# Kernel optimization log

Hardware: AMD Instinct MI355X
Metric: run time of the kernel (lower is better)

The kernel has to match this reference:

```python
import jax, jax.numpy as jnp
import numpy as np

N_CELLS, N_CLASSES, N_GENES, N_EDGES, HID = 100000, 50, 500, 600000, 8
NEG_SLOPE = 0.2  # GATv2Conv default negative_slope


def setup_inputs() -> dict:
    key = jax.random.key(0)
    ks = jax.random.split(key, 10)
    X = jax.random.normal(ks[0], (N_CELLS, N_GENES), jnp.float32)
    Mu = jax.random.normal(ks[1], (N_CLASSES, N_GENES), jnp.float32)
    # variances must be strictly positive
    Var = jax.random.uniform(ks[2], (N_CLASSES, N_GENES), jnp.float32) + 0.5
    W = 0.1 * jax.random.normal(ks[3], (N_CELLS, N_CLASSES), jnp.float32)
    S = 1.0 + 0.05 * jax.random.normal(ks[4], (N_CELLS, 1), jnp.float32)
    edge_index = jax.random.randint(ks[5], (2, N_EDGES), 0, N_CELLS, jnp.int32)
    sc = 1.0 / np.sqrt(N_GENES)
    lin_l_w = sc * jax.random.normal(ks[6], (HID, N_GENES), jnp.float32)
    lin_l_b = jnp.zeros((HID,), jnp.float32)
    lin_r_w = sc * jax.random.normal(ks[7], (HID, N_GENES), jnp.float32)
    lin_r_b = jnp.zeros((HID,), jnp.float32)
    att = jax.random.normal(ks[8], (HID,), jnp.float32) / np.sqrt(HID)
    return dict(X=X, Mu=Mu, Var=Var, W=W, S=S, edge_index=edge_index,
                lin_l_w=lin_l_w, lin_l_b=lin_l_b,
                lin_r_w=lin_r_w, lin_r_b=lin_r_b, att=att)


def _forward(X, Mu, Var, W, S, lin_l_w, lin_l_b, lin_r_w, lin_r_b, att, edge_index):
    N = X.shape[0]
    P = jax.nn.softmax(W, axis=1)  # [N, C]

    # Gaussian log-likelihood term.
    # F[n,c] = -0.5 * sum_g (X[n,g] - Mu[c,g]*S[n])^2 / Var[c,g]
    # Expanded into GEMMs (algebraically identical, avoids the [N,C,G] intermediate):
    invV = 1.0 / Var                          # [C, G]
    t1 = (X * X) @ invV.T                     # [N, C]  sum_g X^2/Var
    t2 = X @ (Mu * invV).T                    # [N, C]  sum_g X*Mu/Var
    t3 = jnp.sum(Mu * Mu * invV, axis=1)      # [C]     sum_g Mu^2/Var
    Fmat = -0.5 * (t1 - 2.0 * S * t2 + (S * S) * t3[None, :])  # [N, C]
    ll_prot = jnp.sum(P * Fmat) / N

    # GATv2 attention coefficients (heads=1, add_self_loops=False).
    gl = X @ lin_l_w.T + lin_l_b              # [N, HID]  lin_l (source side)
    gr = X @ lin_r_w.T + lin_r_b              # [N, HID]  lin_r (target side)
    src, dst = edge_index[0], edge_index[1]
    e = jax.nn.leaky_relu(gl[src] + gr[dst], NEG_SLOPE)  # [E, HID]
    score = e @ att                                       # [E]
    # segment softmax over destination nodes
    m = jax.ops.segment_max(score, dst, num_segments=N)
    ex = jnp.exp(score - m[dst])
    denom = jax.ops.segment_sum(ex, dst, num_segments=N)
    alpha = ex / denom[dst]                               # [E]

    ce_space = -jnp.sum(P[src] * alpha[:, None] * jnp.log(P[dst] + 1e-8)) / N
    return ll_prot, ce_space, P


def reference(X, Mu, Var, W, S, edge_index, lin_l_w, lin_l_b, lin_r_w, lin_r_b, att):
    return _forward(X, Mu, Var, W, S, lin_l_w, lin_l_b, lin_r_w, lin_r_b, att, edge_index)
```

## Files before the change

kernel.cpp:

```cpp
#include <hip/hip_runtime.h>
#include <math.h>

#define N_CELLS   100000
#define N_CLASSES 50
#define N_GENES   500
#define N_EDGES   600000
#define HID       8
#define NKT       8
#define NB_FUSED  1563
#define NB_CE     391

typedef __attribute__((ext_vector_type(4))) float f32x4;
typedef __attribute__((ext_vector_type(8))) short bf16x8;

static const size_t OFF_BF    = 0;
static const size_t OFF_T3    = 147456;
static const size_t OFF_GLR   = 147712;
static const size_t OFF_SCORE = 6547712;
static const size_t OFF_MSEG  = 8947712;
static const size_t OFF_DENOM = 9347712;
static const size_t OFF_NUMER = 9747712;
static const size_t OFF_LLP   = 10147712;
static const size_t OFF_CEP   = 10153968;
static const size_t ZERO_BEG  = OFF_MSEG;
static const size_t ZERO_BYTES= 10147712 - 8947712;

__device__ __forceinline__ ushort f2bf(float f) {
    union { float f; unsigned u; } v; v.f = f;
    unsigned r = v.u + 0x7fffu + ((v.u >> 16) & 1u);
    return (ushort)(r >> 16);
}

__device__ __forceinline__ unsigned cvt_pk_bf16(float lo, float hi) {
    unsigned r;
    asm("v_cvt_pk_bf16_f32 %0, %1, %2" : "=v"(r) : "v"(lo), "v"(hi));
    return r;
}

__device__ __forceinline__ void gload16(const void* g, void* l) {
    __builtin_amdgcn_global_load_lds(
        (const __attribute__((address_space(1))) unsigned int*)g,
        (__attribute__((address_space(3))) unsigned int*)l,
        16, 0, 0);
}

__global__ __launch_bounds__(256) void k_prepB(const float* __restrict__ Var,
                                               const float* __restrict__ Mu,
                                               const float* __restrict__ wl,
                                               const float* __restrict__ wr,
                                               ushort* __restrict__ Bf) {
    int id = blockIdx.x * 256 + threadIdx.x;
    float v = 0.f;
    if (id < 65536) {
        int e    = id & 7;
        int lane = (id >> 3) & 63;
        int j    = (id >> 9) & 15;
        int kt   = id >> 13;
        int t    = j >> 1, ss = j & 1;
        int s    = kt * 2 + ss;
        int k    = s * 32 + ((lane >> 4) << 3) + e;
        int c    = (t & 3) * 16 + (lane & 15);
        if (k < N_GENES && c < N_CLASSES)
            v = (t < 4) ? 1.0f / Var[c * N_GENES + k]
                        : Mu[c * N_GENES + k] / Var[c * N_GENES + k];
    } else {
        int rem  = id - 65536;
        int e    = rem & 7;
        int lane = (rem >> 3) & 63;
        int s    = rem >> 9;
        int k    = s * 32 + ((lane >> 4) << 3) + e;
        int h    = lane & 15;
        if (k < N_GENES)
            v = (h < HID) ? wl[h * N_GENES + k] : wr[(h - HID) * N_GENES + k];
    }
    Bf[id] = f2bf(v);
}

__global__ void k_t3(const float* __restrict__ Var, const float* __restrict__ Mu,
                     float* __restrict__ t3) {
    int c = blockIdx.x;
    int lane = threadIdx.x;
    float s = 0.f;
    for (int g = lane; g < N_GENES; g += 64) {
        float m = Mu[c * N_GENES + g];
        s += m * m / Var[c * N_GENES + g];
    }
    #pragma unroll
    for (int off = 32; off; off >>= 1) s += __shfl_xor(s, off);
    if (lane == 0) t3[c] = s;
}

__global__ __launch_bounds__(256) void k_softmax(const float* __restrict__ W,
                                                 float* __restrict__ P) {
    int wid  = (blockIdx.x * 256 + threadIdx.x) >> 6;
    int lane = threadIdx.x & 63;
    if (wid >= N_CELLS) return;
    float w = (lane < N_CLASSES) ? W[(size_t)wid * N_CLASSES + lane] : -__builtin_inff();
    float m = w;
    #pragma unroll
    for (int off = 32; off; off >>= 1) m = fmaxf(m, __shfl_xor(m, off));
    float e = (lane < N_CLASSES) ? expf(w - m) : 0.f;
    float s = e;
    #pragma unroll
    for (int off = 32; off; off >>= 1) s += __shfl_xor(s, off);
    if (lane < N_CLASSES) P[(size_t)wid * N_CLASSES + lane] = e / s;
}

__global__ __launch_bounds__(256, 1) void k_fused(const float* __restrict__ X,
                                                  const float* __restrict__ S,
                                                  const float* __restrict__ P,
                                                  const ushort* __restrict__ Bf,
                                                  const float* __restrict__ t3,
                                                  const float* __restrict__ bl,
                                                  const float* __restrict__ br,
                                                  float* __restrict__ glr,
                                                  float* __restrict__ llp) {
    __shared__ float  ldsA[2][4][16][16][4];
    __shared__ ushort ldsB[2][16][64][8];
    int tid  = threadIdx.x;
    int lane = tid & 63;
    int wv   = tid >> 6;
    int lhi  = lane >> 4;
    int slot = lane & 15;
    int rbase = blockIdx.x * 64;
    const char* Xc  = (const char*)X;
    const char* Bfc = (const char*)Bf;
    const bf16x8* Bg8 = (const bf16x8*)(Bf + 65536);

    int arow = rbase + wv * 16 + (lane & 15);
    if (arow > N_CELLS - 1) arow = N_CELLS - 1;
    float sv  = S[arow];
    float m2s = -2.0f * sv;

    const f32x4 zz = {0.f, 0.f, 0.f, 0.f};
    f32x4 acc1[4], acc2[4], acc3;
    #pragma unroll
    for (int ct = 0; ct < 4; ++ct) { acc1[ct] = zz; acc2[ct] = zz; }
    acc3 = zz;

    #pragma unroll
    for (int i = 0; i < 4; ++i) {
        int rloc = i * 4 + lhi;
        int row  = rbase + wv * 16 + rloc; if (row > N_CELLS - 1) row = N_CELLS - 1;
        int gi   = slot ^ (rloc & 7); if (gi > 124) gi = 124;
        gload16(Xc + (size_t)row * 2000 + (size_t)gi * 16, &ldsA[0][wv][i * 4][0][0]);
    }
    #pragma unroll
    for (int i = 0; i < 4; ++i) {
        int j = wv * 4 + i;
        gload16(Bfc + (size_t)j * 1024 + (size_t)lane * 16, &ldsB[0][j][0][0]);
    }

    int cur = 0;
    for (int kt = 0; kt < NKT; ++kt) {
        __syncthreads();
        if (kt < NKT - 1) {
            int nxt = cur ^ 1;
            #pragma unroll
            for (int i = 0; i < 4; ++i) {
                int rloc = i * 4 + lhi;
                int row  = rbase + wv * 16 + rloc; if (row > N_CELLS - 1) row = N_CELLS - 1;
                int gi   = (kt + 1) * 16 + (slot ^ (rloc & 7)); if (gi > 124) gi = 124;
                gload16(Xc + (size_t)row * 2000 + (size_t)gi * 16, &ldsA[nxt][wv][i * 4][0][0]);
            }
            #pragma unroll
            for (int i = 0; i < 4; ++i) {
                int j = wv * 4 + i;
                gload16(Bfc + (size_t)(kt + 1) * 16384 + (size_t)j * 1024 + (size_t)lane * 16,
                        &ldsB[nxt][j][0][0]);
            }
        }
        const bf16x8* BL = (const bf16x8*)&ldsB[cur][0][0][0];
        #pragma unroll
        for (int ks = 0; ks < 2; ++ks) {
            int rloc = lane & 15, key = rloc & 7;
            int g8   = ks * 8 + lhi * 2;
            f32x4 xa = *(const f32x4*)&ldsA[cur][wv][rloc][g8 ^ key][0];
            f32x4 xb = *(const f32x4*)&ldsA[cur][wv][rloc][(g8 + 1) ^ key][0];
            union { bf16x8 v; unsigned u[4]; } a1, a2;
            a1.u[0] = cvt_pk_bf16(xa[0] * xa[0], xa[1] * xa[1]);
            a1.u[1] = cvt_pk_bf16(xa[2] * xa[2], xa[3] * xa[3]);
            a1.u[2] = cvt_pk_bf16(xb[0] * xb[0], xb[1] * xb[1]);
            a1.u[3] = cvt_pk_bf16(xb[2] * xb[2], xb[3] * xb[3]);
            a2.u[0] = cvt_pk_bf16(m2s * xa[0], m2s * xa[1]);
            a2.u[1] = cvt_pk_bf16(m2s * xa[2], m2s * xa[3]);
            a2.u[2] = cvt_pk_bf16(m2s * xb[0], m2s * xb[1]);
            a2.u[3] = cvt_pk_bf16(m2s * xb[2], m2s * xb[3]);
            bf16x8 bg = Bg8[(size_t)(kt * 2 + ks) * 64 + lane];
            #pragma unroll
            for (int ct = 0; ct < 4; ++ct)
                acc1[ct] = __builtin_amdgcn_mfma_f32_16x16x32_bf16(a1.v, BL[(ct * 2 + ks) * 64 + lane], acc1[ct], 0, 0, 0);
            #pragma unroll
            for (int ct = 0; ct < 4; ++ct)
                acc2[ct] = __builtin_amdgcn_mfma_f32_16x16x32_bf16(a2.v, BL[((4 + ct) * 2 + ks) * 64 + lane], acc2[ct], 0, 0, 0);
            acc3 = __builtin_amdgcn_mfma_f32_16x16x32_bf16(a2.v, bg, acc3, 0, 0, 0);
        }
        cur ^= 1;
    }

    int col = lane & 15;
    int rg  = lane >> 4;
    float bias = (col < HID) ? bl[col] : br[col - HID];
    float part = 0.f;
    #pragma unroll
    for (int r = 0; r < 4; ++r) {
        int row = rbase + wv * 16 + rg * 4 + r;
        if (row < N_CELLS) {
            float s2 = S[row];
            glr[(size_t)row * 16 + col] = acc3[r] / (-2.0f * s2) + bias;
            float ss = s2 * s2;
            #pragma unroll
            for (int ct = 0; ct < 4; ++ct) {
                int c = ct * 16 + col;
                if (c < N_CLASSES) {
                    float F = -0.5f * (acc1[ct][r] + acc2[ct][r] + ss * t3[c]);
                    part = fmaf(P[(size_t)row * N_CLASSES + c], F, part);
                }
            }
        }
    }
    #pragma unroll
    for (int off = 32; off; off >>= 1) part += __shfl_xor(part, off);
    float* wsum = (float*)&ldsA[0][0][0][0][0];
    __syncthreads();
    if (lane == 0) wsum[wv] = part;
    __syncthreads();
    if (tid == 0) llp[blockIdx.x] = wsum[0] + wsum[1] + wsum[2] + wsum[3];
}

__device__ __forceinline__ unsigned map_f32(float f) {
    int s = __float_as_int(f);
    return (s < 0) ? ~(unsigned)s : ((unsigned)s | 0x80000000u);
}
__device__ __forceinline__ float unmap_f32(unsigned u) {
    return (u & 0x80000000u) ? __int_as_float((int)(u & 0x7fffffffu))
                             : __int_as_float((int)~u);
}

__global__ __launch_bounds__(256) void k_score(const int* __restrict__ ei,
                                               const float* __restrict__ glr,
                                               const float* __restrict__ att,
                                               float* __restrict__ score,
                                               unsigned* __restrict__ mseg) {
    int e = blockIdx.x * 256 + threadIdx.x;
    if (e >= N_EDGES) return;
    int src = ei[e], dst = ei[N_EDGES + e];
    const float4* a = (const float4*)(glr + (size_t)src * 16);
    const float4* b = (const float4*)(glr + (size_t)dst * 16 + 8);
    float4 g0 = a[0], g1 = a[1], h0 = b[0], h1 = b[1];
    const float4* at = (const float4*)att;
    float4 a0 = at[0], a1 = at[1];
    float v, s = 0.f;
    v = g0.x + h0.x; v = v > 0.f ? v : 0.2f * v; s = fmaf(a0.x, v, s);
    v = g0.y + h0.y; v = v > 0.f ? v : 0.2f * v; s = fmaf(a0.y, v, s);
    v = g0.z + h0.z; v = v > 0.f ? v : 0.2f * v; s = fmaf(a0.z, v, s);
    v = g0.w + h0.w; v = v > 0.f ? v : 0.2f * v; s = fmaf(a0.w, v, s);
    v = g1.x + h1.x; v = v > 0.f ? v : 0.2f * v; s = fmaf(a1.x, v, s);
    v = g1.y + h1.y; v = v > 0.f ? v : 0.2f * v; s = fmaf(a1.y, v, s);
    v = g1.z + h1.z; v = v > 0.f ? v : 0.2f * v; s = fmaf(a1.z, v, s);
    v = g1.w + h1.w; v = v > 0.f ? v : 0.2f * v; s = fmaf(a1.w, v, s);
    score[e] = s;
    atomicMax(mseg + dst, map_f32(s));
}

__global__ __launch_bounds__(256) void k_edge2(const int* __restrict__ ei,
                                               const float* __restrict__ score,
                                               const unsigned* __restrict__ mseg,
                                               const float* __restrict__ P,
                                               float* __restrict__ denom,
                                               float* __restrict__ numer) {
    int t = blockIdx.x * 256 + threadIdx.x;
    int e = t >> 4;
    int q = t & 15;
    if (e >= N_EDGES) return;
    int src = ei[e], dst = ei[N_EDGES + e];
    float ex = expf(score[e] - unmap_f32(mseg[dst]));
    const float* Ps = P + (size_t)src * N_CLASSES;
    const float* Pd = P + (size_t)dst * N_CLASSES;
    float v = Ps[q]      * logf(Pd[q]      + 1e-8f)
            + Ps[q + 16] * logf(Pd[q + 16] + 1e-8f)
            + Ps[q + 32] * logf(Pd[q + 32] + 1e-8f);
    if (q < 2) v += Ps[q + 48] * logf(Pd[q + 48] + 1e-8f);
    v += __shfl_xor(v, 8); v += __shfl_xor(v, 4);
    v += __shfl_xor(v, 2); v += __shfl_xor(v, 1);
    if (q == 0) {
        atomicAdd(denom + dst, ex);
        atomicAdd(numer + dst, ex * v);
    }
}

__global__ __launch_bounds__(256) void k_ce(const float* __restrict__ denom,
                                            const float* __restrict__ numer,
                                            float* __restrict__ cep) {
    __shared__ float wsum[4];
    int n = blockIdx.x * 256 + threadIdx.x;
    float v = 0.f;
    if (n < N_CELLS) {
        float d = denom[n];
        v = (d > 0.f) ? numer[n] / d : 0.f;
    }
    #pragma unroll
    for (int off = 32; off; off >>= 1) v += __shfl_xor(v, off);
    if ((threadIdx.x & 63) == 0) wsum[threadIdx.x >> 6] = v;
    __syncthreads();
    if (threadIdx.x == 0) cep[blockIdx.x] = wsum[0] + wsum[1] + wsum[2] + wsum[3];
}

__global__ __launch_bounds__(256) void k_reduce(const float* __restrict__ llp,
                                                const float* __restrict__ cep,
                                                float* __restrict__ out) {
    __shared__ double l1[256], l2[256];
    int t = threadIdx.x;
    double s1 = 0.0, s2 = 0.0;
    for (int i = t; i < NB_FUSED; i += 256) s1 += (double)llp[i];
    for (int i = t; i < NB_CE; i += 256) s2 += (double)cep[i];
    l1[t] = s1; l2[t] = s2;
    __syncthreads();
    for (int off = 128; off; off >>= 1) {
        if (t < off) { l1[t] += l1[t + off]; l2[t] += l2[t + off]; }
        __syncthreads();
    }
    if (t == 0) {
        out[0] = (float)(l1[0] / (double)N_CELLS);
        out[1] = (float)(-l2[0] / (double)N_CELLS);
    }
}

extern "C" void kernel_launch(void* const* d_in, const int* in_sizes, int n_in,
                              void* d_out, int out_size, void* d_ws, size_t ws_size,
                              hipStream_t stream) {
    const float* X   = (const float*)d_in[0];
    const float* Mu  = (const float*)d_in[1];
    const float* Var = (const float*)d_in[2];
    const float* W   = (const float*)d_in[3];
    const float* S   = (const float*)d_in[4];
    const int*   ei  = (const int*)d_in[5];
    const float* wl  = (const float*)d_in[6];
    const float* bl  = (const float*)d_in[7];
    const float* wr  = (const float*)d_in[8];
    const float* br  = (const float*)d_in[9];
    const float* att = (const float*)d_in[10];
    float* out = (float*)d_out;
    char*  ws  = (char*)d_ws;

    ushort*   Bf    = (ushort*)(ws + OFF_BF);
    float*    t3    = (float*)(ws + OFF_T3);
    float*    glr   = (float*)(ws + OFF_GLR);
    float*    score = (float*)(ws + OFF_SCORE);
    unsigned* mseg  = (unsigned*)(ws + OFF_MSEG);
    float*    denom = (float*)(ws + OFF_DENOM);
    float*    numer = (float*)(ws + OFF_NUMER);
    float*    llp   = (float*)(ws + OFF_LLP);
    float*    cep   = (float*)(ws + OFF_CEP);
    float*    P     = out + 2;

    hipMemsetAsync(ws + ZERO_BEG, 0, ZERO_BYTES, stream);

    k_prepB  <<<288, 256, 0, stream>>>(Var, Mu, wl, wr, Bf);
    k_t3     <<<N_CLASSES, 64, 0, stream>>>(Var, Mu, t3);
    k_softmax<<<(N_CELLS * 64 + 255) / 256, 256, 0, stream>>>(W, P);
    k_fused  <<<NB_FUSED, 256, 0, stream>>>(X, S, P, Bf, t3, bl, br, glr, llp);
    k_score  <<<(N_EDGES + 255) / 256, 256, 0, stream>>>(ei, glr, att, score, mseg);
    k_edge2  <<<(N_EDGES * 16 + 255) / 256, 256, 0, stream>>>(ei, score, mseg, P, denom, numer);
    k_ce     <<<NB_CE, 256, 0, stream>>>(denom, numer, cep);
    k_reduce <<<1, 256, 0, stream>>>(llp, cep, out);
}
```

Baseline: 206.1 us.

## Process 32 rows per wave with single-buffered LDS and higher occupancy

Each wave now computes two 16-row tiles (128 rows per block, half as many blocks), so every B fragment read from LDS feeds two MFMAs. The double-buffered LDS prefetch is replaced by a single buffer with load-then-sync each k-step, and launch bounds now ask for 3 blocks per CU so concurrent blocks hide the load latency. The cost is no intra-block overlap of loads and compute, more accumulator registers per thread, and an extra barrier per iteration.

```diff
diff --git a/kernel.cpp b/kernel.cpp
--- a/kernel.cpp
+++ b/kernel.cpp
@@ -7,7 +7,7 @@
 #define N_EDGES   600000
 #define HID       8
 #define NKT       8
-#define NB_FUSED  1563
+#define NB_FUSED  782
 #define NB_CE     391
 
 typedef __attribute__((ext_vector_type(4))) float f32x4;
@@ -106,7 +106,7 @@
     if (lane < N_CLASSES) P[(size_t)wid * N_CLASSES + lane] = e / s;
 }
 
-__global__ __launch_bounds__(256, 1) void k_fused(const float* __restrict__ X,
+__global__ __launch_bounds__(256, 3) void k_fused(const float* __restrict__ X,
                                                   const float* __restrict__ S,
                                                   const float* __restrict__ P,
                                                   const ushort* __restrict__ Bf,
@@ -115,87 +115,91 @@
                                                   const float* __restrict__ br,
                                                   float* __restrict__ glr,
                                                   float* __restrict__ llp) {
-    __shared__ float  ldsA[2][4][16][16][4];
-    __shared__ ushort ldsB[2][16][64][8];
+    __shared__ float  ldsA[4][32][16][4];
+    __shared__ ushort ldsB[16][64][8];
+    __shared__ float  wsum[4];
     int tid  = threadIdx.x;
     int lane = tid & 63;
     int wv   = tid >> 6;
     int lhi  = lane >> 4;
     int slot = lane & 15;
-    int rbase = blockIdx.x * 64;
+    int rbase = blockIdx.x * 128 + wv * 32;
     const char* Xc  = (const char*)X;
     const char* Bfc = (const char*)Bf;
     const bf16x8* Bg8 = (const bf16x8*)(Bf + 65536);
 
-    int arow = rbase + wv * 16 + (lane & 15);
-    if (arow > N_CELLS - 1) arow = N_CELLS - 1;
-    float sv  = S[arow];
-    float m2s = -2.0f * sv;
+    int ar0 = rbase + slot;      if (ar0 > N_CELLS - 1) ar0 = N_CELLS - 1;
+    int ar1 = rbase + 16 + slot; if (ar1 > N_CELLS - 1) ar1 = N_CELLS - 1;
+    float m2s0 = -2.0f * S[ar0];
+    float m2s1 = -2.0f * S[ar1];
 
     const f32x4 zz = {0.f, 0.f, 0.f, 0.f};
-    f32x4 acc1[4], acc2[4], acc3;
-    #pragma unroll
-    for (int ct = 0; ct < 4; ++ct) { acc1[ct] = zz; acc2[ct] = zz; }
-    acc3 = zz;
-
-    #pragma unroll
-    for (int i = 0; i < 4; ++i) {
-        int rloc = i * 4 + lhi;
-        int row  = rbase + wv * 16 + rloc; if (row > N_CELLS - 1) row = N_CELLS - 1;
-        int gi   = slot ^ (rloc & 7); if (gi > 124) gi = 124;
-        gload16(Xc + (size_t)row * 2000 + (size_t)gi * 16, &ldsA[0][wv][i * 4][0][0]);
-    }
-    #pragma unroll
-    for (int i = 0; i < 4; ++i) {
-        int j = wv * 4 + i;
-        gload16(Bfc + (size_t)j * 1024 + (size_t)lane * 16, &ldsB[0][j][0][0]);
-    }
-
-    int cur = 0;
+    f32x4 acc1[2][4], acc2[2][4], acc3[2];
+    #pragma unroll
+    for (int g = 0; g < 2; ++g) {
+        #pragma unroll
+        for (int ct = 0; ct < 4; ++ct) { acc1[g][ct] = zz; acc2[g][ct] = zz; }
+        acc3[g] = zz;
+    }
+
     for (int kt = 0; kt < NKT; ++kt) {
         __syncthreads();
-        if (kt < NKT - 1) {
-            int nxt = cur ^ 1;
+        #pragma unroll
+        for (int i = 0; i < 8; ++i) {
+            int rloc = i * 4 + lhi;
+            int row  = rbase + rloc; if (row > N_CELLS - 1) row = N_CELLS - 1;
+            int gi   = kt * 16 + (slot ^ (rloc & 7)); if (gi > 124) gi = 124;
+            gload16(Xc + (size_t)row * 2000 + (size_t)gi * 16, &ldsA[wv][i * 4][0][0]);
+        }
+        #pragma unroll
+        for (int i = 0; i < 4; ++i) {
+            int j = wv * 4 + i;
+            gload16(Bfc + (size_t)kt * 16384 + (size_t)j * 1024 + (size_t)lane * 16,
+                    &ldsB[j][0][0]);
+        }
+        __syncthreads();
+        const bf16x8* BL = (const bf16x8*)&ldsB[0][0][0];
+        #pragma unroll
+        for (int ks = 0; ks < 2; ++ks) {
+            int key = lane & 7;
+            int c0  = ks * 8 + lhi * 2;
+            f32x4 xa0 = *(const f32x4*)&ldsA[wv][slot][c0 ^ key][0];
+            f32x4 xb0 = *(const f32x4*)&ldsA[wv][slot][(c0 + 1) ^ key][0];
+            f32x4 xa1 = *(const f32x4*)&ldsA[wv][16 + slot][c0 ^ key][0];
+            f32x4 xb1 = *(const f32x4*)&ldsA[wv][16 + slot][(c0 + 1) ^ key][0];
+            union { bf16x8 v; unsigned u[4]; } a1g0, a2g0, a1g1, a2g1;
+            a1g0.u[0] = cvt_pk_bf16(xa0[0] * xa0[0], xa0[1] * xa0[1]);
+            a1g0.u[1] = cvt_pk_bf16(xa0[2] * xa0[2], xa0[3] * xa0[3]);
+            a1g0.u[2] = cvt_pk_bf16(xb0[0] * xb0[0], xb0[1] * xb0[1]);
+            a1g0.u[3] = cvt_pk_bf16(xb0[2] * xb0[2], xb0[3] * xb0[3]);
+            a2g0.u[0] = cvt_pk_bf16(m2s0 * xa0[0], m2s0 * xa0[1]);
+            a2g0.u[1] = cvt_pk_bf16(m2s0 * xa0[2], m2s0 * xa0[3]);
+            a2g0.u[2] = cvt_pk_bf16(m2s0 * xb0[0], m2s0 * xb0[1]);
+            a2g0.u[3] = cvt_pk_bf16(m2s0 * xb0[2], m2s0 * xb0[3]);
+            a1g1.u[0] = cvt_pk_bf16(xa1[0] * xa1[0], xa1[1] * xa1[1]);
+            a1g1.u[1] = cvt_pk_bf16(xa1[2] * xa1[2], xa1[3] * xa1[3]);
+            a1g1.u[2] = cvt_pk_bf16(xb1[0] * xb1[0], xb1[1] * xb1[1]);
+            a1g1.u[3] = cvt_pk_bf16(xb1[2] * xb1[2], xb1[3] * xb1[3]);
+            a2g1.u[0] = cvt_pk_bf16(m2s1 * xa1[0], m2s1 * xa1[1]);
+            a2g1.u[1] = cvt_pk_bf16(m2s1 * xa1[2], m2s1 * xa1[3]);
+            a2g1.u[2] = cvt_pk_bf16(m2s1 * xb1[0], m2s1 * xb1[1]);
+            a2g1.u[3] = cvt_pk_bf16(m2s1 * xb1[2], m2s1 * xb1[3]);
+            bf16x8 bg = Bg8[(size_t)(kt * 2 + ks) * 64 + lane];
             #pragma unroll
-            for (int i = 0; i < 4; ++i) {
-                int rloc = i * 4 + lhi;
-                int row  = rbase + wv * 16 + rloc; if (row > N_CELLS - 1) row = N_CELLS - 1;
-                int gi   = (kt + 1) * 16 + (slot ^ (rloc & 7)); if (gi > 124) gi = 124;
-                gload16(Xc + (size_t)row * 2000 + (size_t)gi * 16, &ldsA[nxt][wv][i * 4][0][0]);
+            for (int ct = 0; ct < 4; ++ct) {
+                bf16x8 b = BL[(ct * 2 + ks) * 64 + lane];
+                acc1[0][ct] = __builtin_amdgcn_mfma_f32_16x16x32_bf16(a1g0.v, b, acc1[0][ct], 0, 0, 0);
+                acc1[1][ct] = __builtin_amdgcn_mfma_f32_16x16x32_bf16(a1g1.v, b, acc1[1][ct], 0, 0, 0);
             }
             #pragma unroll
-            for (int i = 0; i < 4; ++i) {
-                int j = wv * 4 + i;
-                gload16(Bfc + (size_t)(kt + 1) * 16384 + (size_t)j * 1024 + (size_t)lane * 16,
-                        &ldsB[nxt][j][0][0]);
+            for (int ct = 0; ct < 4; ++ct) {
+                bf16x8 b = BL[((4 + ct) * 2 + ks) * 64 + lane];
+                acc2[0][ct] = __builtin_amdgcn_mfma_f32_16x16x32_bf16(a2g0.v, b, acc2[0][ct], 0, 0, 0);
+                acc2[1][ct] = __builtin_amdgcn_mfma_f32_16x16x32_bf16(a2g1.v, b, acc2[1][ct], 0, 0, 0);
             }
+            acc3[0] = __builtin_amdgcn_mfma_f32_16x16x32_bf16(a2g0.v, bg, acc3[0], 0, 0, 0);
+            acc3[1] = __builtin_amdgcn_mfma_f32_16x16x32_bf16(a2g1.v, bg, acc3[1], 0, 0, 0);
         }
-        const bf16x8* BL = (const bf16x8*)&ldsB[cur][0][0][0];
-        #pragma unroll
-        for (int ks = 0; ks < 2; ++ks) {
-            int rloc = lane & 15, key = rloc & 7;
-            int g8   = ks * 8 + lhi * 2;
-            f32x4 xa = *(const f32x4*)&ldsA[cur][wv][rloc][g8 ^ key][0];
-            f32x4 xb = *(const f32x4*)&ldsA[cur][wv][rloc][(g8 + 1) ^ key][0];
-            union { bf16x8 v; unsigned u[4]; } a1, a2;
-            a1.u[0] = cvt_pk_bf16(xa[0] * xa[0], xa[1] * xa[1]);
-            a1.u[1] = cvt_pk_bf16(xa[2] * xa[2], xa[3] * xa[3]);
-            a1.u[2] = cvt_pk_bf16(xb[0] * xb[0], xb[1] * xb[1]);
-            a1.u[3] = cvt_pk_bf16(xb[2] * xb[2], xb[3] * xb[3]);
-            a2.u[0] = cvt_pk_bf16(m2s * xa[0], m2s * xa[1]);
-            a2.u[1] = cvt_pk_bf16(m2s * xa[2], m2s * xa[3]);
-            a2.u[2] = cvt_pk_bf16(m2s * xb[0], m2s * xb[1]);
-            a2.u[3] = cvt_pk_bf16(m2s * xb[2], m2s * xb[3]);
-            bf16x8 bg = Bg8[(size_t)(kt * 2 + ks) * 64 + lane];
-            #pragma unroll
-            for (int ct = 0; ct < 4; ++ct)
-                acc1[ct] = __builtin_amdgcn_mfma_f32_16x16x32_bf16(a1.v, BL[(ct * 2 + ks) * 64 + lane], acc1[ct], 0, 0, 0);
-            #pragma unroll
-            for (int ct = 0; ct < 4; ++ct)
-                acc2[ct] = __builtin_amdgcn_mfma_f32_16x16x32_bf16(a2.v, BL[((4 + ct) * 2 + ks) * 64 + lane], acc2[ct], 0, 0, 0);
-            acc3 = __builtin_amdgcn_mfma_f32_16x16x32_bf16(a2.v, bg, acc3, 0, 0, 0);
-        }
-        cur ^= 1;
     }
 
     int col = lane & 15;
@@ -203,25 +207,27 @@
     float bias = (col < HID) ? bl[col] : br[col - HID];
     float part = 0.f;
     #pragma unroll
-    for (int r = 0; r < 4; ++r) {
-        int row = rbase + wv * 16 + rg * 4 + r;
-        if (row < N_CELLS) {
-            float s2 = S[row];
-            glr[(size_t)row * 16 + col] = acc3[r] / (-2.0f * s2) + bias;
-            float ss = s2 * s2;
-            #pragma unroll
-            for (int ct = 0; ct < 4; ++ct) {
-                int c = ct * 16 + col;
-                if (c < N_CLASSES) {
-                    float F = -0.5f * (acc1[ct][r] + acc2[ct][r] + ss * t3[c]);
-                    part = fmaf(P[(size_t)row * N_CLASSES + c], F, part);
+    for (int g = 0; g < 2; ++g) {
+        #pragma unroll
+        for (int r = 0; r < 4; ++r) {
+            int row = rbase + g * 16 + rg * 4 + r;
+            if (row < N_CELLS) {
+                float s2 = S[row];
+                glr[(size_t)row * 16 + col] = acc3[g][r] / (-2.0f * s2) + bias;
+                float ss = s2 * s2;
+                #pragma unroll
+                for (int ct = 0; ct < 4; ++ct) {
+                    int c = ct * 16 + col;
+                    if (c < N_CLASSES) {
+                        float F = -0.5f * (acc1[g][ct][r] + acc2[g][ct][r] + ss * t3[c]);
+                        part = fmaf(P[(size_t)row * N_CLASSES + c], F, part);
+                    }
                 }
             }
         }
     }
     #pragma unroll
     for (int off = 32; off; off >>= 1) part += __shfl_xor(part, off);
-    float* wsum = (float*)&ldsA[0][0][0][0][0];
     __syncthreads();
     if (lane == 0) wsum[wv] = part;
     __syncthreads();
```

New measurement: 196.3 us. 1.05x faster.

## Stage GAT weight tiles through LDS and pipeline with explicit vmcnt waits

Applied to the files above, without the earlier changes.

The fused GEMM kernel now stages the GATv2 projection weights into shared memory together with the class-weight tiles, instead of reading them from global memory in every k-step. It replaces __syncthreads with raw s_barrier plus a partial s_waitcnt vmcnt and scheduling barriers, so the next tile's async loads stay in flight while the current tile is computed. Launch bounds are raised to allow two blocks per CU for more latency hiding. The cost is extra LDS per block, a hand-counted vmcnt that must match the number of issued loads, and some redundant filler loads for the unused LDS slots.

```diff
diff --git a/kernel.cpp b/kernel.cpp
--- a/kernel.cpp
+++ b/kernel.cpp
@@ -106,7 +106,7 @@
     if (lane < N_CLASSES) P[(size_t)wid * N_CLASSES + lane] = e / s;
 }
 
-__global__ __launch_bounds__(256, 1) void k_fused(const float* __restrict__ X,
+__global__ __launch_bounds__(256, 2) void k_fused(const float* __restrict__ X,
                                                   const float* __restrict__ S,
                                                   const float* __restrict__ P,
                                                   const ushort* __restrict__ Bf,
@@ -116,21 +116,20 @@
                                                   float* __restrict__ glr,
                                                   float* __restrict__ llp) {
     __shared__ float  ldsA[2][4][16][16][4];
-    __shared__ ushort ldsB[2][16][64][8];
+    __shared__ ushort ldsB[2][20][64][8];
+    __shared__ float  wsum[4];
     int tid  = threadIdx.x;
     int lane = tid & 63;
     int wv   = tid >> 6;
     int lhi  = lane >> 4;
     int slot = lane & 15;
-    int rbase = blockIdx.x * 64;
+    int rbase = blockIdx.x * 64 + wv * 16;
     const char* Xc  = (const char*)X;
     const char* Bfc = (const char*)Bf;
-    const bf16x8* Bg8 = (const bf16x8*)(Bf + 65536);
-
-    int arow = rbase + wv * 16 + (lane & 15);
+
+    int arow = rbase + slot;
     if (arow > N_CELLS - 1) arow = N_CELLS - 1;
-    float sv  = S[arow];
-    float m2s = -2.0f * sv;
+    float m2s = -2.0f * S[arow];
 
     const f32x4 zz = {0.f, 0.f, 0.f, 0.f};
     f32x4 acc1[4], acc2[4], acc3;
@@ -138,45 +137,49 @@
     for (int ct = 0; ct < 4; ++ct) { acc1[ct] = zz; acc2[ct] = zz; }
     acc3 = zz;
 
-    #pragma unroll
-    for (int i = 0; i < 4; ++i) {
-        int rloc = i * 4 + lhi;
-        int row  = rbase + wv * 16 + rloc; if (row > N_CELLS - 1) row = N_CELLS - 1;
-        int gi   = slot ^ (rloc & 7); if (gi > 124) gi = 124;
-        gload16(Xc + (size_t)row * 2000 + (size_t)gi * 16, &ldsA[0][wv][i * 4][0][0]);
-    }
-    #pragma unroll
-    for (int i = 0; i < 4; ++i) {
-        int j = wv * 4 + i;
-        gload16(Bfc + (size_t)j * 1024 + (size_t)lane * 16, &ldsB[0][j][0][0]);
-    }
-
-    int cur = 0;
+#define STAGE(KT, BUF) do {                                                        \
+    _Pragma("unroll")                                                              \
+    for (int i = 0; i < 4; ++i) {                                                  \
+        int rloc = i * 4 + lhi;                                                    \
+        int row  = rbase + rloc; if (row > N_CELLS - 1) row = N_CELLS - 1;         \
+        int gi   = (KT) * 16 + (slot ^ (rloc & 7)); if (gi > 124) gi = 124;        \
+        gload16(Xc + (size_t)row * 2000 + (size_t)gi * 16, &ldsA[BUF][wv][i * 4][0][0]); \
+    }                                                                              \
+    _Pragma("unroll")                                                              \
+    for (int i = 0; i < 5; ++i) {                                                  \
+        int j = wv * 5 + i;                                                        \
+        size_t src;                                                                \
+        if (j < 16)      src = (size_t)(KT) * 16384 + (size_t)j * 1024;            \
+        else if (j < 18) src = 131072 + ((size_t)(KT) * 2 + (size_t)(j - 16)) * 1024; \
+        else             src = (size_t)(KT) * 16384;                               \
+        gload16(Bfc + src + (size_t)lane * 16, &ldsB[BUF][j][0][0]);               \
+    }                                                                              \
+} while (0)
+
+    STAGE(0, 0);
+
+    #pragma unroll
     for (int kt = 0; kt < NKT; ++kt) {
-        __syncthreads();
+        const int cur = kt & 1;
         if (kt < NKT - 1) {
-            int nxt = cur ^ 1;
-            #pragma unroll
-            for (int i = 0; i < 4; ++i) {
-                int rloc = i * 4 + lhi;
-                int row  = rbase + wv * 16 + rloc; if (row > N_CELLS - 1) row = N_CELLS - 1;
-                int gi   = (kt + 1) * 16 + (slot ^ (rloc & 7)); if (gi > 124) gi = 124;
-                gload16(Xc + (size_t)row * 2000 + (size_t)gi * 16, &ldsA[nxt][wv][i * 4][0][0]);
-            }
-            #pragma unroll
-            for (int i = 0; i < 4; ++i) {
-                int j = wv * 4 + i;
-                gload16(Bfc + (size_t)(kt + 1) * 16384 + (size_t)j * 1024 + (size_t)lane * 16,
-                        &ldsB[nxt][j][0][0]);
-            }
+            STAGE(kt + 1, cur ^ 1);
+            __builtin_amdgcn_sched_barrier(0);
+            asm volatile("s_waitcnt vmcnt(9)" ::: "memory");
+        } else {
+            __builtin_amdgcn_sched_barrier(0);
+            asm volatile("s_waitcnt vmcnt(0)" ::: "memory");
         }
+        __builtin_amdgcn_sched_barrier(0);
+        __builtin_amdgcn_s_barrier();
+        __builtin_amdgcn_sched_barrier(0);
+
         const bf16x8* BL = (const bf16x8*)&ldsB[cur][0][0][0];
         #pragma unroll
         for (int ks = 0; ks < 2; ++ks) {
-            int rloc = lane & 15, key = rloc & 7;
-            int g8   = ks * 8 + lhi * 2;
-            f32x4 xa = *(const f32x4*)&ldsA[cur][wv][rloc][g8 ^ key][0];
-            f32x4 xb = *(const f32x4*)&ldsA[cur][wv][rloc][(g8 + 1) ^ key][0];
+            int key = slot & 7;
+            int c0  = ks * 8 + lhi * 2;
+            f32x4 xa = *(const f32x4*)&ldsA[cur][wv][slot][c0 ^ key][0];
+            f32x4 xb = *(const f32x4*)&ldsA[cur][wv][slot][(c0 + 1) ^ key][0];
             union { bf16x8 v; unsigned u[4]; } a1, a2;
             a1.u[0] = cvt_pk_bf16(xa[0] * xa[0], xa[1] * xa[1]);
             a1.u[1] = cvt_pk_bf16(xa[2] * xa[2], xa[3] * xa[3]);
@@ -186,7 +189,7 @@
             a2.u[1] = cvt_pk_bf16(m2s * xa[2], m2s * xa[3]);
             a2.u[2] = cvt_pk_bf16(m2s * xb[0], m2s * xb[1]);
             a2.u[3] = cvt_pk_bf16(m2s * xb[2], m2s * xb[3]);
-            bf16x8 bg = Bg8[(size_t)(kt * 2 + ks) * 64 + lane];
+            bf16x8 bg = BL[(16 + ks) * 64 + lane];
             #pragma unroll
             for (int ct = 0; ct < 4; ++ct)
                 acc1[ct] = __builtin_amdgcn_mfma_f32_16x16x32_bf16(a1.v, BL[(ct * 2 + ks) * 64 + lane], acc1[ct], 0, 0, 0);
@@ -195,8 +198,11 @@
                 acc2[ct] = __builtin_amdgcn_mfma_f32_16x16x32_bf16(a2.v, BL[((4 + ct) * 2 + ks) * 64 + lane], acc2[ct], 0, 0, 0);
             acc3 = __builtin_amdgcn_mfma_f32_16x16x32_bf16(a2.v, bg, acc3, 0, 0, 0);
         }
-        cur ^= 1;
-    }
+        __builtin_amdgcn_sched_barrier(0);
+        __builtin_amdgcn_s_barrier();
+        __builtin_amdgcn_sched_barrier(0);
+    }
+#undef STAGE
 
     int col = lane & 15;
     int rg  = lane >> 4;
@@ -204,7 +210,7 @@
     float part = 0.f;
     #pragma unroll
     for (int r = 0; r < 4; ++r) {
-        int row = rbase + wv * 16 + rg * 4 + r;
+        int row = rbase + rg * 4 + r;
         if (row < N_CELLS) {
             float s2 = S[row];
             glr[(size_t)row * 16 + col] = acc3[r] / (-2.0f * s2) + bias;
@@ -221,8 +227,6 @@
     }
     #pragma unroll
     for (int off = 32; off; off >>= 1) part += __shfl_xor(part, off);
-    float* wsum = (float*)&ldsA[0][0][0][0][0];
-    __syncthreads();
     if (lane == 0) wsum[wv] = part;
     __syncthreads();
     if (tid == 0) llp[blockIdx.x] = wsum[0] + wsum[1] + wsum[2] + wsum[3];
```

Measured after the change: 196.2 us. 1.05x faster.
